# Kernel tuning notes

Hardware: AMD Instinct MI355X
Metric: run time of the kernel (lower is better)

The kernel has to match this reference:

```python
import jax, jax.numpy as jnp
import numpy as np

D = 128      # dims[0]: number of nodes
M1 = 256     # dims[1]
M2 = 128     # dims[2]
M3 = 1       # dims[3] (must be 1 for final squeeze)
B = 4096     # batch


def setup_inputs() -> dict:
    key = jax.random.key(0)
    ks = jax.random.split(key, 7)
    x = jax.random.normal(ks[0], (B, D), dtype=jnp.float32)
    # nn.Linear(D, D*M1): weight [D*M1, D], bias [D*M1]
    bnd1 = 1.0 / np.sqrt(D)
    W1 = jax.random.uniform(ks[1], (D * M1, D), minval=-bnd1, maxval=bnd1, dtype=jnp.float32)
    b1 = jax.random.uniform(ks[2], (D * M1,), minval=-bnd1, maxval=bnd1, dtype=jnp.float32)
    # An(D, M1, M2): weight [D, M1, M2], bias [D, M2]
    bnd_a = 1.0 / np.sqrt(M1)
    Wa = jax.random.uniform(ks[3], (D, M1, M2), minval=-bnd_a, maxval=bnd_a, dtype=jnp.float32)
    ba = jax.random.uniform(ks[4], (D, M2), minval=-bnd_a, maxval=bnd_a, dtype=jnp.float32)
    # An(D, M2, M3): weight [D, M2, M3], bias [D, M3]
    bnd_b = 1.0 / np.sqrt(M2)
    Wb = jax.random.uniform(ks[5], (D, M2, M3), minval=-bnd_b, maxval=bnd_b, dtype=jnp.float32)
    bb = jax.random.uniform(ks[6], (D, M3), minval=-bnd_b, maxval=bnd_b, dtype=jnp.float32)
    return {"x": x, "W1": W1, "b1": b1, "Wa": Wa, "ba": ba, "Wb": Wb, "bb": bb}


def reference(x, W1, b1, Wa, ba, Wb, bb):
    # a1: [B, D] -> [B, D*M1] -> [B, D, M1]
    h = (x @ W1.T + b1).reshape(B, D, M1)
    # An layer 1: sigmoid then per-node matmul + bias
    h = jnp.einsum('bni,nio->bno', jax.nn.sigmoid(h), Wa) + ba  # [B, D, M2]
    # An layer 2
    h = jnp.einsum('bni,nio->bno', jax.nn.sigmoid(h), Wb) + bb  # [B, D, 1]
    return h.squeeze(axis=2)  # [B, D]
```

## Files before the change

### kernel.cpp

```cpp
#include <hip/hip_runtime.h>
#include <hip/hip_bf16.h>

#define D_NODES 128
#define KD      128
#define M1_     256
#define M2_     128
#define B_      4096
#define BM      256
#define CI      64
#define NCH     4
#define LOG2E   1.44269504088896f

typedef short bf16x8  __attribute__((ext_vector_type(8)));
typedef short short4v __attribute__((ext_vector_type(4)));
typedef float f32x4   __attribute__((ext_vector_type(4)));
typedef unsigned int uint2v __attribute__((ext_vector_type(2)));

#define MFMA16(a, b, c) __builtin_amdgcn_mfma_f32_16x16x32_bf16((a), (b), (c), 0, 0, 0)

__device__ __forceinline__ short f2b(float f) {
  unsigned u = __builtin_bit_cast(unsigned, f);
  u += 0x7FFFu + ((u >> 16) & 1u);
  return (short)(u >> 16);
}

__device__ __forceinline__ float sigmoid_pre(float acc, float bs) {
  float tt = __builtin_fmaf(acc, -LOG2E, bs);
  float e = __builtin_amdgcn_exp2f(tt);
  return __builtin_amdgcn_rcpf(1.0f + e);
}

__device__ __forceinline__ short4v pack_sig4(f32x4 a, f32x4 bs) {
  float s0 = sigmoid_pre(a[0], bs[0]);
  float s1 = sigmoid_pre(a[1], bs[1]);
  float s2 = sigmoid_pre(a[2], bs[2]);
  float s3 = sigmoid_pre(a[3], bs[3]);
  __hip_bfloat162 h01 = __float22bfloat162_rn(make_float2(s0, s1));
  __hip_bfloat162 h23 = __float22bfloat162_rn(make_float2(s2, s3));
  uint2v uv;
  unsigned u0, u1;
  __builtin_memcpy(&u0, &h01, 4);
  __builtin_memcpy(&u1, &h23, 4);
  uv[0] = u0;
  uv[1] = u1;
  return __builtin_bit_cast(short4v, uv);
}

__global__ void cvt_f2b_k(const float* __restrict__ in, short* __restrict__ out) {
  int i = (blockIdx.x * 256 + threadIdx.x) * 4;
  float4 f = *(const float4*)(in + i);
  short4v s; s[0] = f2b(f.x); s[1] = f2b(f.y); s[2] = f2b(f.z); s[3] = f2b(f.w);
  *(short4v*)(out + i) = s;
}

__global__ void trans_wa_k(const float* __restrict__ Wa, short* __restrict__ waT) {
  __shared__ float lt[64][129];
  int node = blockIdx.x >> 2, iblk = blockIdx.x & 3;
  int t = threadIdx.x;
  for (int j = 0; j < 32; ++j) {
    int e = j * 256 + t;
    int i = e >> 7, o = e & 127;
    lt[i][o] = Wa[(node * M1_ + iblk * 64 + i) * M2_ + o];
  }
  __syncthreads();
  int il = t & 63, ob = t >> 6;
  for (int j = 0; j < 32; ++j) {
    int o = j * 4 + ob;
    waT[(node * M2_ + o) * M1_ + iblk * 64 + il] = f2b(lt[il][o]);
  }
}

template <bool FAST>
__global__ __launch_bounds__(512, 2)
void fused_dag_k(const float* __restrict__ x,  const float* __restrict__ W1,
                 const float* __restrict__ b1, const float* __restrict__ Wa,
                 const float* __restrict__ ba, const float* __restrict__ Wb,
                 const float* __restrict__ bb, float* __restrict__ out,
                 const short* __restrict__ w1b, const short* __restrict__ waT,
                 const short* __restrict__ xb) {
  __shared__ __align__(16) short w1s[M1_ * KD];
  __shared__ __align__(16) short was[M2_ * M1_];
  __shared__ __align__(16) short h1w[8 * 16 * CI];

  int gid = blockIdx.x;
  int xcd = gid & 7, ii = gid >> 3;
  int node = xcd * 16 + (ii >> 4);
  int tile = ii & 15;
  int b0 = tile * BM;

  int t = threadIdx.x;
  int w = t >> 6, l = t & 63;
  int n15 = l & 15, q = l >> 4;

  if (FAST) {
    const short* w1n = w1b + (size_t)node * (M1_ * KD);
    const short* wan = waT + (size_t)node * (M2_ * M1_);
    bf16x8 t1[8], t2[8];
#pragma unroll
    for (int j = 0; j < 8; ++j) t1[j] = *(const bf16x8*)(w1n + (j * 512 + t) * 8);
#pragma unroll
    for (int j = 0; j < 8; ++j) t2[j] = *(const bf16x8*)(wan + (j * 512 + t) * 8);
#pragma unroll
    for (int j = 0; j < 8; ++j) {
      int s = j * 512 + t;
      int row = s >> 4, g = s & 15;
      *(bf16x8*)(&w1s[row * KD + ((g ^ (row & 7)) << 3)]) = t1[j];
    }
#pragma unroll
    for (int j = 0; j < 8; ++j) {
      int s = j * 512 + t;
      int row = s >> 5, g = s & 31;
      *(bf16x8*)(&was[row * M1_ + ((g ^ (row & 7)) << 3)]) = t2[j];
    }
  } else {
#pragma unroll
    for (int j = 0; j < 8; ++j) {
      int s = j * 512 + t;
      int row = s >> 4, g = s & 15;
      const float* src = W1 + ((size_t)node * M1_ + row) * KD + g * 8;
      float4 f0 = *(const float4*)(src);
      float4 f1 = *(const float4*)(src + 4);
      bf16x8 v;
      v[0] = f2b(f0.x); v[1] = f2b(f0.y); v[2] = f2b(f0.z); v[3] = f2b(f0.w);
      v[4] = f2b(f1.x); v[5] = f2b(f1.y); v[6] = f2b(f1.z); v[7] = f2b(f1.w);
      *(bf16x8*)(&w1s[row * KD + ((g ^ (row & 7)) << 3)]) = v;
    }
    for (int j = 0; j < 8; ++j) {
      int s = j * 512 + t;
      int o = s >> 5, g = s & 31;
      bf16x8 v;
#pragma unroll
      for (int e = 0; e < 8; ++e)
        v[e] = f2b(Wa[((size_t)node * M1_ + g * 8 + e) * M2_ + o]);
      *(bf16x8*)(&was[o * M1_ + ((g ^ (o & 7)) << 3)]) = v;
    }
  }

  bf16x8 xa[2][4];
  {
    int rb = b0 + w * 32;
#pragma unroll
    for (int mt = 0; mt < 2; ++mt) {
      int row = rb + mt * 16 + n15;
#pragma unroll
      for (int kk = 0; kk < 4; ++kk) {
        int k0 = kk * 32 + q * 8;
        if (FAST) {
          xa[mt][kk] = *(const bf16x8*)(xb + row * KD + k0);
        } else {
          float4 f0 = *(const float4*)(x + row * KD + k0);
          float4 f1 = *(const float4*)(x + row * KD + k0 + 4);
          bf16x8 v;
          v[0] = f2b(f0.x); v[1] = f2b(f0.y); v[2] = f2b(f0.z); v[3] = f2b(f0.w);
          v[4] = f2b(f1.x); v[5] = f2b(f1.y); v[6] = f2b(f1.z); v[7] = f2b(f1.w);
          xa[mt][kk] = v;
        }
      }
    }
  }

  __syncthreads();

  int swz = n15 & 7;
  int hsw = (swz >> 2) << 6;
  int qx16 = (q ^ (swz & 3)) << 4;
  int swd32 = (swz >> 1) << 5;
  int qhx = ((q >> 1) ^ (swz & 1)) << 4;
  int qlo8 = (q & 1) << 3;

  const char* w1c8 = (const char*)w1s;
  const char* wac8 = (const char*)was;
  char* h1c8 = (char*)h1w;

  int w1o = n15 * 256 + qx16 + hsw;
  int wao = n15 * 512 + qx16 + hsw;
  int h1wo = w * 2048 + n15 * 128 + qlo8 + qhx + swd32;
  int h1ro = w * 2048 + n15 * 128 + qx16 + hsw;

  f32x4 acc2[2][8];
#pragma unroll
  for (int a = 0; a < 2; ++a)
#pragma unroll
    for (int b = 0; b < 8; ++b) acc2[a][b] = (f32x4){0.f, 0.f, 0.f, 0.f};

  for (int c = 0; c < NCH; ++c) {
    bf16x8 wa[8][2];
    int wabase = wao + c * 128;
#pragma unroll
    for (int kk = 0; kk < 2; ++kk) {
      int p = wabase ^ (kk << 6);
#pragma unroll
      for (int ot = 0; ot < 8; ++ot)
        wa[ot][kk] = *(const bf16x8*)(wac8 + p + ot * 8192);
    }

    const float* b1c = b1 + node * M1_ + c * CI;
    f32x4 bs[4];
#pragma unroll
    for (int it = 0; it < 4; ++it)
      bs[it] = (*(const f32x4*)(b1c + it * 16 + q * 4)) * (-LOG2E);

    f32x4 acc1[4][2];
#pragma unroll
    for (int a = 0; a < 4; ++a) {
      acc1[a][0] = (f32x4){0.f, 0.f, 0.f, 0.f};
      acc1[a][1] = (f32x4){0.f, 0.f, 0.f, 0.f};
    }
    int w1base = w1o + c * 16384;
#pragma unroll
    for (int kk = 0; kk < 4; ++kk) {
      int p = w1base ^ (kk << 6);
#pragma unroll
      for (int it = 0; it < 4; ++it) {
        bf16x8 wf = *(const bf16x8*)(w1c8 + p + it * 4096);
        acc1[it][0] = MFMA16(wf, xa[0][kk], acc1[it][0]);
        acc1[it][1] = MFMA16(wf, xa[1][kk], acc1[it][1]);
      }
    }

    short4v s4a[4], s4b[4];
#pragma unroll
    for (int it = 0; it < 4; ++it) s4a[it] = pack_sig4(acc1[it][0], bs[it]);
#pragma unroll
    for (int it = 0; it < 4; ++it)
      *(short4v*)(h1c8 + (h1wo ^ (it << 5))) = s4a[it];
#pragma unroll
    for (int it = 0; it < 4; ++it) s4b[it] = pack_sig4(acc1[it][1], bs[it]);

    bf16x8 ha0[2];
#pragma unroll
    for (int kk = 0; kk < 2; ++kk)
      ha0[kk] = *(const bf16x8*)(h1c8 + (h1ro ^ (kk << 6)));
#pragma unroll
    for (int kk = 0; kk < 2; ++kk)
#pragma unroll
      for (int ot = 0; ot < 8; ++ot)
        acc2[0][ot] = MFMA16(ha0[kk], wa[ot][kk], acc2[0][ot]);

#pragma unroll
    for (int it = 0; it < 4; ++it)
      *(short4v*)(h1c8 + (h1wo ^ (it << 5))) = s4b[it];

    bf16x8 ha1[2];
#pragma unroll
    for (int kk = 0; kk < 2; ++kk)
      ha1[kk] = *(const bf16x8*)(h1c8 + (h1ro ^ (kk << 6)));
#pragma unroll
    for (int kk = 0; kk < 2; ++kk)
#pragma unroll
      for (int ot = 0; ot < 8; ++ot)
        acc2[1][ot] = MFMA16(ha1[kk], wa[ot][kk], acc2[1][ot]);
  }

  const float* ban = ba + node * M2_;
  const float* wbn = Wb + node * M2_;
  float bbv = bb[node];
  float bas[8], wbs[8];
#pragma unroll
  for (int ot = 0; ot < 8; ++ot) {
    int o = ot * 16 + n15;
    bas[ot] = ban[o] * (-LOG2E);
    wbs[ot] = wbn[o];
  }
#pragma unroll
  for (int mt = 0; mt < 2; ++mt) {
    f32x4 rs = (f32x4){0.f, 0.f, 0.f, 0.f};
#pragma unroll
    for (int ot = 0; ot < 8; ++ot)
#pragma unroll
      for (int r = 0; r < 4; ++r)
        rs[r] += sigmoid_pre(acc2[mt][ot][r], bas[ot]) * wbs[ot];
#pragma unroll
    for (int r = 0; r < 4; ++r) {
      float v = rs[r];
      v += __shfl_xor(v, 1);
      v += __shfl_xor(v, 2);
      v += __shfl_xor(v, 4);
      v += __shfl_xor(v, 8);
      if (n15 == 0)
        out[(size_t)(b0 + w * 32 + mt * 16 + q * 4 + r) * D_NODES + node] = v + bbv;
    }
  }
}

extern "C" void kernel_launch(void* const* d_in, const int* in_sizes, int n_in,
                              void* d_out, int out_size, void* d_ws, size_t ws_size,
                              hipStream_t stream) {
  const float* x  = (const float*)d_in[0];
  const float* W1 = (const float*)d_in[1];
  const float* b1 = (const float*)d_in[2];
  const float* Wa = (const float*)d_in[3];
  const float* ba = (const float*)d_in[4];
  const float* Wb = (const float*)d_in[5];
  const float* bb = (const float*)d_in[6];
  float* out = (float*)d_out;

  const size_t W1_ELEMS = (size_t)D_NODES * M1_ * KD;
  const size_t WA_ELEMS = (size_t)D_NODES * M1_ * M2_;
  const size_t X_ELEMS  = (size_t)B_ * KD;
  const size_t NEED = (W1_ELEMS + WA_ELEMS + X_ELEMS) * sizeof(short);

  const int GRID = D_NODES * (B_ / BM);

  if (ws_size >= NEED) {
    short* w1b = (short*)d_ws;
    short* waT = w1b + W1_ELEMS;
    short* xb  = waT + WA_ELEMS;
    cvt_f2b_k<<<(int)(W1_ELEMS / 1024), 256, 0, stream>>>(W1, w1b);
    cvt_f2b_k<<<(int)(X_ELEMS / 1024), 256, 0, stream>>>(x, xb);
    trans_wa_k<<<D_NODES * 4, 256, 0, stream>>>(Wa, waT);
    fused_dag_k<true><<<GRID, 512, 0, stream>>>(x, W1, b1, Wa, ba, Wb, bb, out,
                                                w1b, waT, xb);
  } else {
    fused_dag_k<false><<<GRID, 512, 0, stream>>>(x, W1, b1, Wa, ba, Wb, bb, out,
                                                 nullptr, nullptr, nullptr);
  }
}
```

Baseline: 125.9 us.

## Halve block to 4 waves with 64 rows each, hoisting W1 fragments into registers

Each block now runs 256 threads (4 waves), and each wave handles 64 batch rows instead of 32, so the per-node weights in LDS are reused across more rows per wave. W1 fragments for a chunk are loaded once into registers and reused across four m-tiles, and the layer-1 MFMA for the next m-tile is interleaved with the sigmoid/layer-2 work of the current one. This cuts LDS reads of W1 and aims to overlap the MFMA and ALU work. In exchange it raises register pressure (wf, xa and acc2 all grow), halves the waves available per block, and doubles the per-thread weight staging loads.

Result: slower. 155.5 us (+23.6%).

```diff
diff --git a/kernel.cpp b/kernel.cpp
--- a/kernel.cpp
+++ b/kernel.cpp
@@ -7,6 +7,7 @@
 #define M2_     128
 #define B_      4096
 #define BM      256
+#define WROWS   64
 #define CI      64
 #define NCH     4
 #define LOG2E   1.44269504088896f
@@ -71,7 +72,7 @@
 }
 
 template <bool FAST>
-__global__ __launch_bounds__(512, 2)
+__global__ __launch_bounds__(256, 1)
 void fused_dag_k(const float* __restrict__ x,  const float* __restrict__ W1,
                  const float* __restrict__ b1, const float* __restrict__ Wa,
                  const float* __restrict__ ba, const float* __restrict__ Wb,
@@ -80,7 +81,7 @@
                  const short* __restrict__ xb) {
   __shared__ __align__(16) short w1s[M1_ * KD];
   __shared__ __align__(16) short was[M2_ * M1_];
-  __shared__ __align__(16) short h1w[8 * 16 * CI];
+  __shared__ __align__(16) short h1w[4 * 16 * CI];
 
   int gid = blockIdx.x;
   int xcd = gid & 7, ii = gid >> 3;
@@ -95,27 +96,27 @@
   if (FAST) {
     const short* w1n = w1b + (size_t)node * (M1_ * KD);
     const short* wan = waT + (size_t)node * (M2_ * M1_);
-    bf16x8 t1[8], t2[8];
-#pragma unroll
-    for (int j = 0; j < 8; ++j) t1[j] = *(const bf16x8*)(w1n + (j * 512 + t) * 8);
-#pragma unroll
-    for (int j = 0; j < 8; ++j) t2[j] = *(const bf16x8*)(wan + (j * 512 + t) * 8);
-#pragma unroll
-    for (int j = 0; j < 8; ++j) {
-      int s = j * 512 + t;
+    bf16x8 t1[16], t2[16];
+#pragma unroll
+    for (int j = 0; j < 16; ++j) t1[j] = *(const bf16x8*)(w1n + (j * 256 + t) * 8);
+#pragma unroll
+    for (int j = 0; j < 16; ++j) t2[j] = *(const bf16x8*)(wan + (j * 256 + t) * 8);
+#pragma unroll
+    for (int j = 0; j < 16; ++j) {
+      int s = j * 256 + t;
       int row = s >> 4, g = s & 15;
       *(bf16x8*)(&w1s[row * KD + ((g ^ (row & 7)) << 3)]) = t1[j];
     }
 #pragma unroll
-    for (int j = 0; j < 8; ++j) {
-      int s = j * 512 + t;
+    for (int j = 0; j < 16; ++j) {
+      int s = j * 256 + t;
       int row = s >> 5, g = s & 31;
       *(bf16x8*)(&was[row * M1_ + ((g ^ (row & 7)) << 3)]) = t2[j];
     }
   } else {
 #pragma unroll
-    for (int j = 0; j < 8; ++j) {
-      int s = j * 512 + t;
+    for (int j = 0; j < 16; ++j) {
+      int s = j * 256 + t;
       int row = s >> 4, g = s & 15;
       const float* src = W1 + ((size_t)node * M1_ + row) * KD + g * 8;
       float4 f0 = *(const float4*)(src);
@@ -125,8 +126,8 @@
       v[4] = f2b(f1.x); v[5] = f2b(f1.y); v[6] = f2b(f1.z); v[7] = f2b(f1.w);
       *(bf16x8*)(&w1s[row * KD + ((g ^ (row & 7)) << 3)]) = v;
     }
-    for (int j = 0; j < 8; ++j) {
-      int s = j * 512 + t;
+    for (int j = 0; j < 16; ++j) {
+      int s = j * 256 + t;
       int o = s >> 5, g = s & 31;
       bf16x8 v;
 #pragma unroll
@@ -136,11 +137,11 @@
     }
   }
 
-  bf16x8 xa[2][4];
+  bf16x8 xa[4][4];
   {
-    int rb = b0 + w * 32;
-#pragma unroll
-    for (int mt = 0; mt < 2; ++mt) {
+    int rb = b0 + w * WROWS;
+#pragma unroll
+    for (int mt = 0; mt < 4; ++mt) {
       int row = rb + mt * 16 + n15;
 #pragma unroll
       for (int kk = 0; kk < 4; ++kk) {
@@ -177,13 +178,24 @@
   int h1wo = w * 2048 + n15 * 128 + qlo8 + qhx + swd32;
   int h1ro = w * 2048 + n15 * 128 + qx16 + hsw;
 
-  f32x4 acc2[2][8];
-#pragma unroll
-  for (int a = 0; a < 2; ++a)
+  f32x4 acc2[4][8];
+#pragma unroll
+  for (int a = 0; a < 4; ++a)
 #pragma unroll
     for (int b = 0; b < 8; ++b) acc2[a][b] = (f32x4){0.f, 0.f, 0.f, 0.f};
 
+  const float* b1n = b1 + node * M1_;
+
   for (int c = 0; c < NCH; ++c) {
+    bf16x8 wf[4][4];
+    int w1base = w1o + c * 16384;
+#pragma unroll
+    for (int kk = 0; kk < 4; ++kk) {
+      int p = w1base ^ (kk << 6);
+#pragma unroll
+      for (int it = 0; it < 4; ++it)
+        wf[it][kk] = *(const bf16x8*)(w1c8 + p + it * 4096);
+    }
     bf16x8 wa[8][2];
     int wabase = wao + c * 128;
 #pragma unroll
@@ -194,62 +206,50 @@
         wa[ot][kk] = *(const bf16x8*)(wac8 + p + ot * 8192);
     }
 
-    const float* b1c = b1 + node * M1_ + c * CI;
+    const float* b1c = b1n + c * CI;
     f32x4 bs[4];
 #pragma unroll
     for (int it = 0; it < 4; ++it)
       bs[it] = (*(const f32x4*)(b1c + it * 16 + q * 4)) * (-LOG2E);
 
-    f32x4 acc1[4][2];
-#pragma unroll
-    for (int a = 0; a < 4; ++a) {
-      acc1[a][0] = (f32x4){0.f, 0.f, 0.f, 0.f};
-      acc1[a][1] = (f32x4){0.f, 0.f, 0.f, 0.f};
-    }
-    int w1base = w1o + c * 16384;
-#pragma unroll
-    for (int kk = 0; kk < 4; ++kk) {
-      int p = w1base ^ (kk << 6);
-#pragma unroll
-      for (int it = 0; it < 4; ++it) {
-        bf16x8 wf = *(const bf16x8*)(w1c8 + p + it * 4096);
-        acc1[it][0] = MFMA16(wf, xa[0][kk], acc1[it][0]);
-        acc1[it][1] = MFMA16(wf, xa[1][kk], acc1[it][1]);
+    f32x4 acc1[4];
+#pragma unroll
+    for (int a = 0; a < 4; ++a) acc1[a] = (f32x4){0.f, 0.f, 0.f, 0.f};
+#pragma unroll
+    for (int kk = 0; kk < 4; ++kk)
+#pragma unroll
+      for (int it = 0; it < 4; ++it)
+        acc1[it] = MFMA16(wf[it][kk], xa[0][kk], acc1[it]);
+
+#pragma unroll
+    for (int mt = 0; mt < 4; ++mt) {
+      short4v s4[4];
+#pragma unroll
+      for (int it = 0; it < 4; ++it) s4[it] = pack_sig4(acc1[it], bs[it]);
+#pragma unroll
+      for (int it = 0; it < 4; ++it)
+        *(short4v*)(h1c8 + (h1wo ^ (it << 5))) = s4[it];
+      bf16x8 ha[2];
+#pragma unroll
+      for (int kk = 0; kk < 2; ++kk)
+        ha[kk] = *(const bf16x8*)(h1c8 + (h1ro ^ (kk << 6)));
+
+      if (mt < 3) {
+#pragma unroll
+        for (int a = 0; a < 4; ++a) acc1[a] = (f32x4){0.f, 0.f, 0.f, 0.f};
+#pragma unroll
+        for (int kk = 0; kk < 4; ++kk)
+#pragma unroll
+          for (int it = 0; it < 4; ++it)
+            acc1[it] = MFMA16(wf[it][kk], xa[mt + 1][kk], acc1[it]);
       }
-    }
-
-    short4v s4a[4], s4b[4];
-#pragma unroll
-    for (int it = 0; it < 4; ++it) s4a[it] = pack_sig4(acc1[it][0], bs[it]);
-#pragma unroll
-    for (int it = 0; it < 4; ++it)
-      *(short4v*)(h1c8 + (h1wo ^ (it << 5))) = s4a[it];
-#pragma unroll
-    for (int it = 0; it < 4; ++it) s4b[it] = pack_sig4(acc1[it][1], bs[it]);
-
-    bf16x8 ha0[2];
-#pragma unroll
-    for (int kk = 0; kk < 2; ++kk)
-      ha0[kk] = *(const bf16x8*)(h1c8 + (h1ro ^ (kk << 6)));
-#pragma unroll
-    for (int kk = 0; kk < 2; ++kk)
-#pragma unroll
-      for (int ot = 0; ot < 8; ++ot)
-        acc2[0][ot] = MFMA16(ha0[kk], wa[ot][kk], acc2[0][ot]);
-
-#pragma unroll
-    for (int it = 0; it < 4; ++it)
-      *(short4v*)(h1c8 + (h1wo ^ (it << 5))) = s4b[it];
-
-    bf16x8 ha1[2];
-#pragma unroll
-    for (int kk = 0; kk < 2; ++kk)
-      ha1[kk] = *(const bf16x8*)(h1c8 + (h1ro ^ (kk << 6)));
-#pragma unroll
-    for (int kk = 0; kk < 2; ++kk)
-#pragma unroll
-      for (int ot = 0; ot < 8; ++ot)
-        acc2[1][ot] = MFMA16(ha1[kk], wa[ot][kk], acc2[1][ot]);
+
+#pragma unroll
+      for (int kk = 0; kk < 2; ++kk)
+#pragma unroll
+        for (int ot = 0; ot < 8; ++ot)
+          acc2[mt][ot] = MFMA16(ha[kk], wa[ot][kk], acc2[mt][ot]);
+    }
   }
 
   const float* ban = ba + node * M2_;
@@ -263,7 +263,7 @@
     wbs[ot] = wbn[o];
   }
 #pragma unroll
-  for (int mt = 0; mt < 2; ++mt) {
+  for (int mt = 0; mt < 4; ++mt) {
     f32x4 rs = (f32x4){0.f, 0.f, 0.f, 0.f};
 #pragma unroll
     for (int ot = 0; ot < 8; ++ot)
@@ -278,7 +278,7 @@
       v += __shfl_xor(v, 4);
       v += __shfl_xor(v, 8);
       if (n15 == 0)
-        out[(size_t)(b0 + w * 32 + mt * 16 + q * 4 + r) * D_NODES + node] = v + bbv;
+        out[(size_t)(b0 + w * WROWS + mt * 16 + q * 4 + r) * D_NODES + node] = v + bbv;
     }
   }
 }
@@ -309,10 +309,10 @@
     cvt_f2b_k<<<(int)(W1_ELEMS / 1024), 256, 0, stream>>>(W1, w1b);
     cvt_f2b_k<<<(int)(X_ELEMS / 1024), 256, 0, stream>>>(x, xb);
     trans_wa_k<<<D_NODES * 4, 256, 0, stream>>>(Wa, waT);
-    fused_dag_k<true><<<GRID, 512, 0, stream>>>(x, W1, b1, Wa, ba, Wb, bb, out,
+    fused_dag_k<true><<<GRID, 256, 0, stream>>>(x, W1, b1, Wa, ba, Wb, bb, out,
                                                 w1b, waT, xb);
   } else {
-    fused_dag_k<false><<<GRID, 512, 0, stream>>>(x, W1, b1, Wa, ba, Wb, bb, out,
+    fused_dag_k<false><<<GRID, 256, 0, stream>>>(x, W1, b1, Wa, ba, Wb, bb, out,
                                                  nullptr, nullptr, nullptr);
   }
 }
```

## Stagger chunk order and m-tile order across waves, raise priority around MFMA blocks

Applied to the files above, without the earlier changes.

Odd waves now start the M1 chunk loop at a different offset, and they process the two m-subtiles in the opposite order from even waves. The intent is to desynchronise neighbouring waves so their MFMA bursts and their sigmoid/LDS phases interleave on the SIMD instead of colliding. s_setprio is raised around each MFMA block so matrix work gets issue priority. The cost is a branch into two template instantiations, which increases code size, and priority toggling that may not help if the waves are already interleaved.

Result: slower. 133.3 us (+5.9%).

```diff
diff --git a/kernel.cpp b/kernel.cpp
--- a/kernel.cpp
+++ b/kernel.cpp
@@ -17,6 +17,8 @@
 typedef unsigned int uint2v __attribute__((ext_vector_type(2)));
 
 #define MFMA16(a, b, c) __builtin_amdgcn_mfma_f32_16x16x32_bf16((a), (b), (c), 0, 0, 0)
+
+template <int V> struct IC { static constexpr int v = V; };
 
 __device__ __forceinline__ short f2b(float f) {
   unsigned u = __builtin_bit_cast(unsigned, f);
@@ -183,7 +185,11 @@
 #pragma unroll
     for (int b = 0; b < 8; ++b) acc2[a][b] = (f32x4){0.f, 0.f, 0.f, 0.f};
 
-  for (int c = 0; c < NCH; ++c) {
+  int codd = (w & 1) << 1;
+
+  for (int cc = 0; cc < NCH; ++cc) {
+    int c = (cc + codd) & 3;
+
     bf16x8 wa[8][2];
     int wabase = wao + c * 128;
 #pragma unroll
@@ -207,6 +213,7 @@
       acc1[a][1] = (f32x4){0.f, 0.f, 0.f, 0.f};
     }
     int w1base = w1o + c * 16384;
+    __builtin_amdgcn_s_setprio(1);
 #pragma unroll
     for (int kk = 0; kk < 4; ++kk) {
       int p = w1base ^ (kk << 6);
@@ -217,39 +224,50 @@
         acc1[it][1] = MFMA16(wf, xa[1][kk], acc1[it][1]);
       }
     }
-
-    short4v s4a[4], s4b[4];
-#pragma unroll
-    for (int it = 0; it < 4; ++it) s4a[it] = pack_sig4(acc1[it][0], bs[it]);
-#pragma unroll
-    for (int it = 0; it < 4; ++it)
-      *(short4v*)(h1c8 + (h1wo ^ (it << 5))) = s4a[it];
-#pragma unroll
-    for (int it = 0; it < 4; ++it) s4b[it] = pack_sig4(acc1[it][1], bs[it]);
-
-    bf16x8 ha0[2];
-#pragma unroll
-    for (int kk = 0; kk < 2; ++kk)
-      ha0[kk] = *(const bf16x8*)(h1c8 + (h1ro ^ (kk << 6)));
-#pragma unroll
-    for (int kk = 0; kk < 2; ++kk)
-#pragma unroll
-      for (int ot = 0; ot < 8; ++ot)
-        acc2[0][ot] = MFMA16(ha0[kk], wa[ot][kk], acc2[0][ot]);
-
-#pragma unroll
-    for (int it = 0; it < 4; ++it)
-      *(short4v*)(h1c8 + (h1wo ^ (it << 5))) = s4b[it];
-
-    bf16x8 ha1[2];
-#pragma unroll
-    for (int kk = 0; kk < 2; ++kk)
-      ha1[kk] = *(const bf16x8*)(h1c8 + (h1ro ^ (kk << 6)));
-#pragma unroll
-    for (int kk = 0; kk < 2; ++kk)
-#pragma unroll
-      for (int ot = 0; ot < 8; ++ot)
-        acc2[1][ot] = MFMA16(ha1[kk], wa[ot][kk], acc2[1][ot]);
+    __builtin_amdgcn_s_setprio(0);
+
+    auto mts = [&](auto tag) {
+      constexpr int mA = decltype(tag)::v;
+      constexpr int mB = 1 - mA;
+      short4v s4a[4], s4b[4];
+#pragma unroll
+      for (int it = 0; it < 4; ++it) s4a[it] = pack_sig4(acc1[it][mA], bs[it]);
+#pragma unroll
+      for (int it = 0; it < 4; ++it)
+        *(short4v*)(h1c8 + (h1wo ^ (it << 5))) = s4a[it];
+#pragma unroll
+      for (int it = 0; it < 4; ++it) s4b[it] = pack_sig4(acc1[it][mB], bs[it]);
+
+      bf16x8 haA[2];
+#pragma unroll
+      for (int kk = 0; kk < 2; ++kk)
+        haA[kk] = *(const bf16x8*)(h1c8 + (h1ro ^ (kk << 6)));
+      __builtin_amdgcn_s_setprio(1);
+#pragma unroll
+      for (int kk = 0; kk < 2; ++kk)
+#pragma unroll
+        for (int ot = 0; ot < 8; ++ot)
+          acc2[mA][ot] = MFMA16(haA[kk], wa[ot][kk], acc2[mA][ot]);
+      __builtin_amdgcn_s_setprio(0);
+
+#pragma unroll
+      for (int it = 0; it < 4; ++it)
+        *(short4v*)(h1c8 + (h1wo ^ (it << 5))) = s4b[it];
+
+      bf16x8 haB[2];
+#pragma unroll
+      for (int kk = 0; kk < 2; ++kk)
+        haB[kk] = *(const bf16x8*)(h1c8 + (h1ro ^ (kk << 6)));
+      __builtin_amdgcn_s_setprio(1);
+#pragma unroll
+      for (int kk = 0; kk < 2; ++kk)
+#pragma unroll
+        for (int ot = 0; ot < 8; ++ot)
+          acc2[mB][ot] = MFMA16(haB[kk], wa[ot][kk], acc2[mB][ot]);
+      __builtin_amdgcn_s_setprio(0);
+    };
+    if (w & 1) mts(IC<1>{});
+    else       mts(IC<0>{});
   }
 
   const float* ban = ba + node * M2_;
```
